# Kernel tuning notes

Measured on AMD Instinct MI355X. Metric: run time of the kernel, lower is better.

## Reference

```python
import jax, jax.numpy as jnp
import numpy as np

N = 20000      # nodes
E = 300000     # edges
HID = 128
HEADS = 4
DH = HID // HEADS
NF = 4         # node_features
EF = 3         # edge_features
NS = 10        # num_servers (Q-head output)
NL = 4         # num_layers


def _ln(h, g, b):
    m = h.mean(-1, keepdims=True)
    v = ((h - m) ** 2).mean(-1, keepdims=True)
    return (h - m) / jnp.sqrt(v + 1e-5) * g + b


def _lrelu(h):
    return jnp.where(h >= 0, h, 0.2 * h)


def setup_inputs() -> dict:
    key = jax.random.key(0)
    ks = jax.random.split(key, 48)
    it = iter(range(48))

    def W(shape, fan_in):
        return jax.random.normal(ks[next(it)], shape, jnp.float32) / np.float32(np.sqrt(fan_in))

    inp = {}
    inp["x"] = jax.random.normal(ks[next(it)], (N, NF), jnp.float32)
    inp["edge_index"] = jax.random.randint(ks[next(it)], (2, E), 0, N)
    inp["edge_attr"] = jax.random.normal(ks[next(it)], (E, EF), jnp.float32)
    # node / edge encoders
    inp["ne_w"] = W((NF, HID), NF); inp["ne_b"] = jnp.zeros((HID,), jnp.float32)
    inp["ne_g"] = jnp.ones((HID,), jnp.float32); inp["ne_beta"] = jnp.zeros((HID,), jnp.float32)
    inp["ee_w"] = W((EF, HID), EF); inp["ee_b"] = jnp.zeros((HID,), jnp.float32)
    inp["ee_g"] = jnp.ones((HID,), jnp.float32); inp["ee_beta"] = jnp.zeros((HID,), jnp.float32)
    # EdgeConv layers (stacked over NL)
    inp["ec_w1"] = W((NL, 2 * HID, HID), 2 * HID); inp["ec_b1"] = jnp.zeros((NL, HID), jnp.float32)
    inp["ec_lng"] = jnp.ones((NL, HID), jnp.float32); inp["ec_lnb"] = jnp.zeros((NL, HID), jnp.float32)
    inp["ec_w2"] = W((NL, HID, HID), HID); inp["ec_b2"] = jnp.zeros((NL, HID), jnp.float32)
    inp["ec_wa"] = W((NL, 2 * HID, 1), 2 * HID); inp["ec_ba"] = jnp.zeros((NL, 1), jnp.float32)
    # GATConv layers
    inp["gat_w"] = W((NL, HID, HID), HID)
    inp["gat_asrc"] = W((NL, HEADS, DH), DH)
    inp["gat_adst"] = W((NL, HEADS, DH), DH)
    inp["gat_bias"] = jnp.zeros((NL, HID), jnp.float32)
    # post-block layer norms
    inp["ln_g"] = jnp.ones((NL, HID), jnp.float32); inp["ln_b"] = jnp.zeros((NL, HID), jnp.float32)
    # dueling heads
    inp["adv_w1"] = W((HID, HID), HID); inp["adv_b1"] = jnp.zeros((HID,), jnp.float32)
    inp["adv_g"] = jnp.ones((HID,), jnp.float32); inp["adv_beta"] = jnp.zeros((HID,), jnp.float32)
    inp["adv_w2"] = W((HID, NS), HID); inp["adv_b2"] = jnp.zeros((NS,), jnp.float32)
    inp["val_w1"] = W((HID, HID), HID); inp["val_b1"] = jnp.zeros((HID,), jnp.float32)
    inp["val_g"] = jnp.ones((HID,), jnp.float32); inp["val_beta"] = jnp.zeros((HID,), jnp.float32)
    inp["val_w2"] = W((HID, 1), HID); inp["val_b2"] = jnp.zeros((1,), jnp.float32)
    return inp


def _forward(x, edge_attr, edge_index,
             ne_w, ne_b, ne_g, ne_beta, ee_w, ee_b, ee_g, ee_beta,
             ec_w1, ec_b1, ec_lng, ec_lnb, ec_w2, ec_b2, ec_wa, ec_ba,
             gat_w, gat_asrc, gat_adst, gat_bias, ln_g, ln_b,
             adv_w1, adv_b1, adv_g, adv_beta, adv_w2, adv_b2,
             val_w1, val_b1, val_g, val_beta, val_w2, val_b2):
    src = edge_index[0]
    dst = edge_index[1]
    h = _ln(_lrelu(x @ ne_w + ne_b), ne_g, ne_beta)                 # node encoder (eval: no dropout)
    _ea = _ln(_lrelu(edge_attr @ ee_w + ee_b), ee_g, ee_beta)        # edge encoder; message() only tests presence
    deg = jax.ops.segment_sum(jnp.ones((E,), h.dtype), dst, num_segments=N)  # in-degree [N]
    sl = jnp.arange(N)
    src_sl = jnp.concatenate([src, sl])                              # GATConv adds self-loops
    dst_sl = jnp.concatenate([dst, sl])

    xc = h
    res = h
    for i in range(NL):
        # ---- EdgeConv: gather-concat, per-edge MLP, sigmoid edge-attention gate, scatter ----
        tmp = jnp.concatenate([xc[dst], xc[src]], axis=1)            # [E, 2H] = x_i || x_j
        m = _lrelu(tmp @ ec_w1[i] + ec_b1[i])
        m = _ln(m, ec_lng[i], ec_lnb[i])
        m = _lrelu(m @ ec_w2[i] + ec_b2[i])
        gate = jax.nn.sigmoid(tmp @ ec_wa[i] + ec_ba[i])             # [E, 1]
        msg = m * gate
        if i % 2 == 0:  # 'max' aggregation (PyG fills isolated nodes with 0)
            agg = jax.ops.segment_max(msg, dst, num_segments=N)
            agg = jnp.where(deg[:, None] > 0, agg, 0.0)
        else:           # 'mean'
            agg = jax.ops.segment_sum(msg, dst, num_segments=N) / jnp.maximum(deg, 1.0)[:, None]
        # ---- GATConv (self-loops, segment softmax over destination) ----
        wx = (xc @ gat_w[i]).reshape(N, HEADS, DH)
        asrc = (wx * gat_asrc[i]).sum(-1)                            # [N, HEADS]
        adst = (wx * gat_adst[i]).sum(-1)
        e = _lrelu(asrc[src_sl] + adst[dst_sl])                      # [E+N, HEADS]
        emax = jax.ops.segment_max(e, dst_sl, num_segments=N)
        p = jnp.exp(e - emax[dst_sl])
        den = jax.ops.segment_sum(p, dst_sl, num_segments=N)
        alpha = p / den[dst_sl]                                      # attention (eval: no dropout)
        gat_out = jax.ops.segment_sum(alpha[:, :, None] * wx[src_sl], dst_sl, num_segments=N)
        gat_out = gat_out.reshape(N, HID) + gat_bias[i]
        # ---- residual + norm + activation ----
        xc = _lrelu(_ln(res + agg + gat_out, ln_g[i], ln_b[i]))
        res = xc

    t = xc[0]                                                        # task node representation
    a = _ln(_lrelu(t @ adv_w1 + adv_b1), adv_g, adv_beta)
    a = a @ adv_w2 + adv_b2                                          # [NS]
    v = _ln(_lrelu(t @ val_w1 + val_b1), val_g, val_beta)
    v = v @ val_w2 + val_b2                                          # [1]
    q = v + (a - a.mean())
    return q, v


def reference(x, edge_index, edge_attr,
              ne_w, ne_b, ne_g, ne_beta, ee_w, ee_b, ee_g, ee_beta,
              ec_w1, ec_b1, ec_lng, ec_lnb, ec_w2, ec_b2, ec_wa, ec_ba,
              gat_w, gat_asrc, gat_adst, gat_bias, ln_g, ln_b,
              adv_w1, adv_b1, adv_g, adv_beta, adv_w2, adv_b2,
              val_w1, val_b1, val_g, val_beta, val_w2, val_b2):
    return _forward(x, edge_attr, edge_index,
                    ne_w, ne_b, ne_g, ne_beta, ee_w, ee_b, ee_g, ee_beta,
                    ec_w1, ec_b1, ec_lng, ec_lnb, ec_w2, ec_b2, ec_wa, ec_ba,
                    gat_w, gat_asrc, gat_adst, gat_bias, ln_g, ln_b,
                    adv_w1, adv_b1, adv_g, adv_beta, adv_w2, adv_b2,
                    val_w1, val_b1, val_g, val_beta, val_w2, val_b2)
```

## Files before the change

kernel.cpp:

```cpp
#include <hip/hip_runtime.h>
#include <hip/hip_bf16.h>

#define NN 20000
#define NE 300000
#define HIDN 128
#define NLAY 4

typedef short short8 __attribute__((ext_vector_type(8)));
typedef float f32x4 __attribute__((ext_vector_type(4)));
typedef unsigned short us16;
typedef unsigned int u32;

__device__ __forceinline__ float lrelu(float x){ return x >= 0.f ? x : 0.2f * x; }
__device__ __forceinline__ float b2f(us16 u){ return __uint_as_float(((u32)u) << 16); }
__device__ __forceinline__ us16 f2b(float f){
    u32 u = __float_as_uint(f);
    u += 0x7FFFu + ((u >> 16) & 1u);
    return (us16)(u >> 16);
}
__device__ __forceinline__ float rawf(const void* p, size_t i, int dt){
    return dt ? b2f(((const us16*)p)[i]) : ((const float*)p)[i];
}
__device__ __forceinline__ int swzi(int i){
    return (i & ~15) | ((i & 15) ^ (((i >> 5) & 3) << 2));
}

__device__ __forceinline__ void ln_stats_128(float v, volatile float* red, float& mean, float& inv){
    float s = v, s2 = v * v;
#pragma unroll
    for (int m = 32; m >= 1; m >>= 1){ s += __shfl_xor(s, m, 64); s2 += __shfl_xor(s2, m, 64); }
    int w = threadIdx.x >> 6;
    if ((threadIdx.x & 63) == 0){ red[w*2] = s; red[w*2+1] = s2; }
    __syncthreads();
    float ts = red[0] + red[2], ts2 = red[1] + red[3];
    mean = ts * (1.f/128.f);
    float var = ts2 * (1.f/128.f) - mean * mean;
    inv = rsqrtf(var + 1e-5f);
    __syncthreads();
}

__global__ void k_detect(const u32* __restrict__ ne_g, int* __restrict__ flag){
    flag[0] = (ne_g[0] == 0x3F803F80u) ? 1 : 0;
}

struct ConvEnt { const void* s; float* d; int n; int pad; };
struct ConvTab { ConvEnt c[28]; int cnt; int pad[3]; };

__global__ void k_convert_all(ConvTab tab, const int* __restrict__ flag){
    int ti = blockIdx.y;
    if (ti >= tab.cnt) return;
    const void* s = tab.c[ti].s;
    float* d = tab.c[ti].d;
    int n = tab.c[ti].n;
    int dt = flag[0];
    for (int i = blockIdx.x*blockDim.x + threadIdx.x; i < n; i += gridDim.x*blockDim.x)
        d[i] = rawf(s, i, dt);
}

#define W1SZ (8*144*32)
#define W2SZ (4*128*32)
#define PER_L (W1SZ + 2*W2SZ)
#define PTOT2 (NLAY*PER_L)
__global__ void k_prepw(const void* __restrict__ ecw1r, const void* __restrict__ ecwar,
                        const void* __restrict__ ecw2r, const void* __restrict__ gatwr,
                        const int* __restrict__ flag,
                        us16* __restrict__ w1s, us16* __restrict__ w2s, us16* __restrict__ gws){
    int id = blockIdx.x*blockDim.x + threadIdx.x;
    if (id >= PTOT2) return;
    int dt = flag[0];
    int L = id / PER_L, r = id % PER_L;
    if (r < W1SZ){
        int kk = r / 4608, rem = r % 4608, n = rem >> 5, ks = rem & 31;
        int k = kk*32 + ks;
        float v;
        if (n < 128)      v = rawf(ecw1r, (size_t)L*32768 + (size_t)k*128 + n, dt);
        else if (n == 128) v = rawf(ecwar, (size_t)L*256 + k, dt);
        else               v = 0.f;
        w1s[(size_t)L*W1SZ + r] = f2b(v);
    } else if (r < W1SZ + W2SZ){
        int rr = r - W1SZ;
        int kk = rr >> 12, rem = rr & 4095, n = rem >> 5, ks = rem & 31;
        int k = kk*32 + ks;
        w2s[(size_t)L*W2SZ + rr] = f2b(rawf(ecw2r, (size_t)L*16384 + (size_t)k*128 + n, dt));
    } else {
        int rr = r - W1SZ - W2SZ;
        int kk = rr >> 12, rem = rr & 4095, n = rem >> 5, ks = rem & 31;
        int k = kk*32 + ks;
        gws[(size_t)L*W2SZ + rr] = f2b(rawf(gatwr, (size_t)L*16384 + (size_t)k*128 + n, dt));
    }
}

__global__ void k_hist(const int* __restrict__ dstI, int* __restrict__ cnt){
    int e = blockIdx.x*blockDim.x + threadIdx.x;
    if (e < NE) atomicAdd(&cnt[dstI[e]], 1);
}
__global__ void k_scan(const int* __restrict__ cnt, int* __restrict__ rowptr){
    __shared__ int ps[256];
    int t = threadIdx.x;
    int chunk = (NN + 255) / 256;
    int beg = t*chunk, end = beg + chunk; if (end > NN) end = NN;
    int s = 0;
    for (int i = beg; i < end; ++i) s += cnt[i];
    ps[t] = s; __syncthreads();
    int off = 0;
    for (int i = 0; i < t; ++i) off += ps[i];
    int run = off;
    for (int i = beg; i < end; ++i){ rowptr[i] = run; run += cnt[i]; }
    if (t == 255) rowptr[NN] = run;
}
__global__ void k_csrfill(const int* __restrict__ srcI, const int* __restrict__ dstI,
                          int* __restrict__ cur, int* __restrict__ perm,
                          int* __restrict__ csr_src){
    int e = blockIdx.x*blockDim.x + threadIdx.x;
    if (e < NE){
        int p = atomicAdd(&cur[dstI[e]], 1);
        perm[e] = p;
        csr_src[p] = srcI[e];
    }
}

__global__ void k_nodeenc(const float* __restrict__ xf, const float* __restrict__ w,
                          const float* __restrict__ b, const float* __restrict__ g,
                          const float* __restrict__ beta, float* __restrict__ h,
                          us16* __restrict__ xb){
    __shared__ float red[4];
    int n = blockIdx.x, t = threadIdx.x;
    float acc = b[t];
#pragma unroll
    for (int k = 0; k < 4; ++k) acc = fmaf(xf[n*4+k], w[k*HIDN+t], acc);
    acc = lrelu(acc);
    float mean, inv; ln_stats_128(acc, red, mean, inv);
    float o = (acc-mean)*inv*g[t] + beta[t];
    h[(size_t)n*HIDN+t] = o;
    xb[(size_t)n*HIDN+t] = f2b(o);
}

__global__ __launch_bounds__(256, 3) void k_edgeconv_mfma(
    const us16* __restrict__ xb, const int* __restrict__ srcI, const int* __restrict__ dstI,
    const us16* __restrict__ w1s, const us16* __restrict__ w2s,
    const float* __restrict__ b1, const float* __restrict__ lng, const float* __restrict__ lnb,
    const float* __restrict__ b2, const float* __restrict__ baP,
    const int* __restrict__ perm, us16* __restrict__ msg)
{
    __shared__ __align__(16) us16 m1s[128*128];
    __shared__ __align__(16) u32 bsl[2][2304];
    int t = threadIdx.x;
    int wv = t >> 6, lane = t & 63, g = lane >> 4, lr = lane & 15;
    int e0 = blockIdx.x * 128;

    u32 offd[2], offs[2];
#pragma unroll
    for (int m = 0; m < 2; ++m){
        int le = e0 + wv*32 + m*16 + lr; if (le >= NE) le = NE - 1;
        offd[m] = (u32)dstI[le] * HIDN;
        offs[m] = (u32)srcI[le] * HIDN;
    }

    const u32* w1u = (const u32*)w1s;
    const u32* w2u = (const u32*)w2s;

    f32x4 acc[2][9];
#pragma unroll
    for (int m = 0; m < 2; ++m)
#pragma unroll
        for (int nt = 0; nt < 9; ++nt) acc[m][nt] = (f32x4)(0.f);

    u32 rS[9];
#pragma unroll
    for (int q = 0; q < 9; ++q) rS[q] = w1u[t + 256*q];
#pragma unroll
    for (int q = 0; q < 9; ++q) bsl[0][swzi(t + 256*q)] = rS[q];
#pragma unroll
    for (int q = 0; q < 9; ++q) rS[q] = w1u[2304 + t + 256*q];
    short8 aCur[2], aNxt[2];
#pragma unroll
    for (int m = 0; m < 2; ++m)
        aCur[m] = *(const short8*)(xb + offd[m] + g*8);
    __syncthreads();

#pragma unroll
    for (int kk = 0; kk < 8; ++kk){
        if (kk < 7){
            int kn = kk + 1;
#pragma unroll
            for (int m = 0; m < 2; ++m)
                aNxt[m] = *(const short8*)(xb + ((kn < 4) ? offd[m] : offs[m]) + (kn&3)*32 + g*8);
        }
        const us16* bp = (const us16*)bsl[kk & 1];
#pragma unroll
        for (int nt = 0; nt < 9; ++nt){
            int row = nt*16 + lr;
            short8 bF = *(const short8*)(bp + row*32 + (g*8 ^ (((row>>1)&3)<<3)));
            acc[0][nt] = __builtin_amdgcn_mfma_f32_16x16x32_bf16(aCur[0], bF, acc[0][nt], 0, 0, 0);
            acc[1][nt] = __builtin_amdgcn_mfma_f32_16x16x32_bf16(aCur[1], bF, acc[1][nt], 0, 0, 0);
        }
        if (kk < 7){
#pragma unroll
            for (int q = 0; q < 9; ++q) bsl[(kk+1)&1][swzi(t + 256*q)] = rS[q];
            if (kk < 6){
#pragma unroll
                for (int q = 0; q < 9; ++q) rS[q] = w1u[(kk+2)*2304 + t + 256*q];
            }
        }
        aCur[0] = aNxt[0]; aCur[1] = aNxt[1];
        __syncthreads();
    }

    float ba = baP[0];
    float ga[2][4];
#pragma unroll
    for (int m = 0; m < 2; ++m)
#pragma unroll
        for (int r = 0; r < 4; ++r){
            float gv = 1.f / (1.f + __expf(-(acc[m][8][r] + ba)));
            ga[m][r] = __shfl(gv, lane & 48, 64);
        }

    float b1v[8], lngv[8], lnbv[8];
#pragma unroll
    for (int nt = 0; nt < 8; ++nt){
        int c = nt*16 + lr;
        b1v[nt] = b1[c]; lngv[nt] = lng[c]; lnbv[nt] = lnb[c];
    }

    u32 rS2[8];
#pragma unroll
    for (int q = 0; q < 8; ++q) rS2[q] = w2u[t + 256*q];

#pragma unroll
    for (int m = 0; m < 2; ++m){
        float m1v[8][4];
        float s1[4] = {0,0,0,0}, s2[4] = {0,0,0,0};
#pragma unroll
        for (int nt = 0; nt < 8; ++nt)
#pragma unroll
            for (int r = 0; r < 4; ++r){
                float v = lrelu(acc[m][nt][r] + b1v[nt]);
                m1v[nt][r] = v; s1[r] += v; s2[r] += v*v;
            }
#pragma unroll
        for (int mk = 8; mk >= 1; mk >>= 1)
#pragma unroll
            for (int r = 0; r < 4; ++r){ s1[r] += __shfl_xor(s1[r], mk, 64); s2[r] += __shfl_xor(s2[r], mk, 64); }
#pragma unroll
        for (int r = 0; r < 4; ++r){
            float mean = s1[r] * (1.f/128.f);
            float var  = s2[r] * (1.f/128.f) - mean*mean;
            float inv  = rsqrtf(var + 1e-5f);
            int row = wv*32 + m*16 + g*4 + r;
            int swz = (row & 7) << 3;
#pragma unroll
            for (int nt = 0; nt < 8; ++nt){
                float v = (m1v[nt][r] - mean)*inv*lngv[nt] + lnbv[nt];
                m1s[row*128 + ((nt*16 + lr) ^ swz)] = f2b(v);
            }
        }
    }
    __syncthreads();
#pragma unroll
    for (int q = 0; q < 8; ++q) bsl[0][swzi(t + 256*q)] = rS2[q];
#pragma unroll
    for (int q = 0; q < 8; ++q) rS2[q] = w2u[2048 + t + 256*q];
    __syncthreads();

    f32x4 acc2[2][8];
#pragma unroll
    for (int m = 0; m < 2; ++m)
#pragma unroll
        for (int nt = 0; nt < 8; ++nt) acc2[m][nt] = (f32x4)(0.f);
#pragma unroll
    for (int kk = 0; kk < 4; ++kk){
        const us16* bp = (const us16*)bsl[kk & 1];
        short8 aF[2];
#pragma unroll
        for (int m = 0; m < 2; ++m){
            int arow = wv*32 + m*16 + lr;
            int aswz = (arow & 7) << 3;
            aF[m] = *(const short8*)(m1s + arow*128 + ((kk*32 + g*8) ^ aswz));
        }
#pragma unroll
        for (int nt = 0; nt < 8; ++nt){
            int row = nt*16 + lr;
            short8 bF = *(const short8*)(bp + row*32 + (g*8 ^ (((row>>1)&3)<<3)));
            acc2[0][nt] = __builtin_amdgcn_mfma_f32_16x16x32_bf16(aF[0], bF, acc2[0][nt], 0, 0, 0);
            acc2[1][nt] = __builtin_amdgcn_mfma_f32_16x16x32_bf16(aF[1], bF, acc2[1][nt], 0, 0, 0);
        }
        if (kk < 3){
#pragma unroll
            for (int q = 0; q < 8; ++q) bsl[(kk+1)&1][swzi(t + 256*q)] = rS2[q];
            if (kk < 2){
#pragma unroll
                for (int q = 0; q < 8; ++q) rS2[q] = w2u[(kk+2)*2048 + t + 256*q];
            }
        }
        __syncthreads();
    }

    float b2v[8];
#pragma unroll
    for (int nt = 0; nt < 8; ++nt) b2v[nt] = b2[nt*16 + lr];
#pragma unroll
    for (int m = 0; m < 2; ++m)
#pragma unroll
        for (int r = 0; r < 4; ++r){
            int row = wv*32 + m*16 + g*4 + r;
            int swz = (row & 7) << 3;
#pragma unroll
            for (int nt = 0; nt < 8; ++nt){
                float v = lrelu(acc2[m][nt][r] + b2v[nt]) * ga[m][r];
                m1s[row*128 + ((nt*16 + lr) ^ swz)] = f2b(v);
            }
        }
    __syncthreads();
    {
        int row = t >> 1, half = t & 1;
        int e = e0 + row;
        if (e < NE){
            size_t ob = (size_t)perm[e] * HIDN;
            int swz = (row & 7) << 3;
#pragma unroll
            for (int q = 0; q < 8; ++q){
                int col = half*64 + q*8;
                *(short8*)(msg + ob + col) = *(const short8*)(m1s + row*128 + (col ^ swz));
            }
        }
    }
}

__global__ __launch_bounds__(256, 4) void k_gatwx(
    const us16* __restrict__ xb, const us16* __restrict__ gws,
    const float* __restrict__ aws, const float* __restrict__ awd,
    us16* __restrict__ wxb, float* __restrict__ asrc, float* __restrict__ adst)
{
    __shared__ __align__(16) us16 sbuf[64*128];
    __shared__ __align__(16) u32 bsl[2][2048];
    int t = threadIdx.x;
    int wv = t >> 6, lane = t & 63, g = lane >> 4, lr = lane & 15;
    int n0 = blockIdx.x * 64;

    int rn = n0 + wv*16 + lr; if (rn >= NN) rn = NN - 1;
    short8 aN[4];
#pragma unroll
    for (int kk = 0; kk < 4; ++kk)
        aN[kk] = *(const short8*)(xb + (size_t)rn*HIDN + kk*32 + g*8);

    const u32* gwu = (const u32*)gws;
    u32 rS[8];
#pragma unroll
    for (int q = 0; q < 8; ++q) rS[q] = gwu[t + 256*q];
#pragma unroll
    for (int q = 0; q < 8; ++q) bsl[0][swzi(t + 256*q)] = rS[q];
#pragma unroll
    for (int q = 0; q < 8; ++q) rS[q] = gwu[2048 + t + 256*q];
    __syncthreads();

    f32x4 acc[8];
#pragma unroll
    for (int i = 0; i < 8; ++i) acc[i] = (f32x4)(0.f);
#pragma unroll
    for (int kk = 0; kk < 4; ++kk){
        const us16* bp = (const us16*)bsl[kk & 1];
#pragma unroll
        for (int nt = 0; nt < 8; ++nt){
            int row = nt*16 + lr;
            short8 bF = *(const short8*)(bp + row*32 + (g*8 ^ (((row>>1)&3)<<3)));
            acc[nt] = __builtin_amdgcn_mfma_f32_16x16x32_bf16(aN[kk], bF, acc[nt], 0, 0, 0);
        }
        if (kk < 3){
#pragma unroll
            for (int q = 0; q < 8; ++q) bsl[(kk+1)&1][swzi(t + 256*q)] = rS[q];
            if (kk < 2){
#pragma unroll
                for (int q = 0; q < 8; ++q) rS[q] = gwu[(kk+2)*2048 + t + 256*q];
            }
        }
        __syncthreads();
    }

    float awsv[8], awdv[8];
#pragma unroll
    for (int nt = 0; nt < 8; ++nt){ awsv[nt] = aws[nt*16 + lr]; awdv[nt] = awd[nt*16 + lr]; }
    float sa[4][4], sd[4][4];
#pragma unroll
    for (int r = 0; r < 4; ++r)
#pragma unroll
        for (int h = 0; h < 4; ++h){
            sa[r][h] = acc[2*h][r]*awsv[2*h] + acc[2*h+1][r]*awsv[2*h+1];
            sd[r][h] = acc[2*h][r]*awdv[2*h] + acc[2*h+1][r]*awdv[2*h+1];
        }
#pragma unroll
    for (int mk = 8; mk >= 1; mk >>= 1)
#pragma unroll
        for (int r = 0; r < 4; ++r)
#pragma unroll
            for (int h = 0; h < 4; ++h){
                sa[r][h] += __shfl_xor(sa[r][h], mk, 64);
                sd[r][h] += __shfl_xor(sd[r][h], mk, 64);
            }
    if (lr == 0){
#pragma unroll
        for (int r = 0; r < 4; ++r){
            int n = n0 + wv*16 + g*4 + r;
            if (n < NN){
                float4 va = make_float4(sa[r][0], sa[r][1], sa[r][2], sa[r][3]);
                float4 vd = make_float4(sd[r][0], sd[r][1], sd[r][2], sd[r][3]);
                *(float4*)(asrc + (size_t)n*4) = va;
                *(float4*)(adst + (size_t)n*4) = vd;
            }
        }
    }

#pragma unroll
    for (int r = 0; r < 4; ++r){
        int row = wv*16 + g*4 + r;
        int swz = (row & 7) << 3;
#pragma unroll
        for (int nt = 0; nt < 8; ++nt)
            sbuf[row*128 + ((nt*16 + lr) ^ swz)] = f2b(acc[nt][r]);
    }
    __syncthreads();
    {
        int row = t >> 2, ch = t & 3;
        int n = n0 + row;
        if (n < NN){
            int swz = (row & 7) << 3;
#pragma unroll
            for (int q = 0; q < 4; ++q){
                int col = ch*32 + q*8;
                *(short8*)(wxb + (size_t)n*HIDN + col) = *(const short8*)(sbuf + row*128 + (col ^ swz));
            }
        }
    }
}

__global__ __launch_bounds__(256, 8) void k_node_update(
    const int* __restrict__ rowptr, const int* __restrict__ csr_src,
    const us16* __restrict__ msg, const us16* __restrict__ wxb,
    const float* __restrict__ asrc, const float* __restrict__ adst,
    const float* __restrict__ xc, const float* __restrict__ gbias,
    const float* __restrict__ lng, const float* __restrict__ lnb,
    float* __restrict__ xout, us16* __restrict__ xbout, int maxmode)
{
    int wv = threadIdx.x >> 6, l = threadIdx.x & 63;
    int n = blockIdx.x*4 + wv;
    if (n >= NN) return;
    int c0 = 2*l, c1 = 2*l + 1;
    int h = l >> 4;

    int b = rowptr[n], en = rowptr[n+1];
    int deg = en - b;

    float adst_h = adst[(size_t)n*4 + h];
    float pself = __expf(fminf(lrelu(asrc[(size_t)n*4 + h] + adst_h), 80.f));
    u32 wq = *(const u32*)(wxb + (size_t)n*HIDN + c0);
    float att0 = pself * b2f((us16)(wq & 0xFFFFu));
    float att1 = pself * b2f((us16)(wq >> 16));
    float den = pself;

    float agg0, agg1;
    if (maxmode){ agg0 = agg1 = -3.0e38f; } else { agg0 = agg1 = 0.f; }

    for (int i = b; i < en; ++i){
        int s = csr_src[i];
        u32 mq = *(const u32*)(msg + (size_t)i*HIDN + c0);
        float m0 = b2f((us16)(mq & 0xFFFFu)), m1 = b2f((us16)(mq >> 16));
        if (maxmode){ agg0 = fmaxf(agg0, m0); agg1 = fmaxf(agg1, m1); }
        else        { agg0 += m0; agg1 += m1; }
        float p = __expf(fminf(lrelu(asrc[(size_t)s*4 + h] + adst_h), 80.f));
        u32 wq2 = *(const u32*)(wxb + (size_t)s*HIDN + c0);
        att0 = fmaf(p, b2f((us16)(wq2 & 0xFFFFu)), att0);
        att1 = fmaf(p, b2f((us16)(wq2 >> 16)), att1);
        den += p;
    }
    float rden = 1.f / den;
    att0 *= rden; att1 *= rden;
    if (maxmode){ if (deg == 0){ agg0 = 0.f; agg1 = 0.f; } }
    else { float rd = 1.f / fmaxf((float)deg, 1.f); agg0 *= rd; agg1 *= rd; }

    float2 xcv = *(const float2*)(xc + (size_t)n*HIDN + c0);
    float s0 = xcv.x + agg0 + att0 + gbias[c0];
    float s1 = xcv.y + agg1 + att1 + gbias[c1];

    float ss = s0 + s1, ss2 = s0*s0 + s1*s1;
#pragma unroll
    for (int mk = 32; mk >= 1; mk >>= 1){ ss += __shfl_xor(ss, mk, 64); ss2 += __shfl_xor(ss2, mk, 64); }
    float mean = ss * (1.f/128.f);
    float var  = ss2 * (1.f/128.f) - mean*mean;
    float inv  = rsqrtf(var + 1e-5f);
    float o0 = lrelu((s0-mean)*inv*lng[c0] + lnb[c0]);
    float o1 = lrelu((s1-mean)*inv*lng[c1] + lnb[c1]);
    *(float2*)(xout + (size_t)n*HIDN + c0) = make_float2(o0, o1);
    u32 pk = (u32)f2b(o0) | ((u32)f2b(o1) << 16);
    *(u32*)(xbout + (size_t)n*HIDN + c0) = pk;
}

__global__ void k_heads(const float* __restrict__ xc,
                        const float* __restrict__ aw1, const float* __restrict__ ab1,
                        const float* __restrict__ ag,  const float* __restrict__ abeta,
                        const float* __restrict__ aw2, const float* __restrict__ ab2,
                        const float* __restrict__ vw1, const float* __restrict__ vb1,
                        const float* __restrict__ vg,  const float* __restrict__ vbeta,
                        const float* __restrict__ vw2, const float* __restrict__ vb2,
                        void* __restrict__ dout, const int* __restrict__ flag){
    __shared__ float red[4];
    __shared__ float ts[128], u1[128], aout[10];
    int t = threadIdx.x;
    ts[t] = xc[t];
    __syncthreads();
    float acc = ab1[t];
    for (int k = 0; k < 128; ++k) acc = fmaf(ts[k], aw1[k*HIDN+t], acc);
    acc = lrelu(acc);
    float mean, inv; ln_stats_128(acc, red, mean, inv);
    u1[t] = (acc-mean)*inv*ag[t] + abeta[t];
    __syncthreads();
    if (t < 10){
        float a = ab2[t];
        for (int k = 0; k < 128; ++k) a = fmaf(u1[k], aw2[k*10+t], a);
        aout[t] = a;
    }
    __syncthreads();
    float accv = vb1[t];
    for (int k = 0; k < 128; ++k) accv = fmaf(ts[k], vw1[k*HIDN+t], accv);
    accv = lrelu(accv);
    float meanv, invv; ln_stats_128(accv, red, meanv, invv);
    float v1 = (accv-meanv)*invv*vg[t] + vbeta[t];
    float pv = v1 * vw2[t];
#pragma unroll
    for (int m = 32; m >= 1; m >>= 1) pv += __shfl_xor(pv, m, 64);
    if ((t & 63) == 0) red[t >> 6] = pv;
    __syncthreads();
    if (t == 0){
        float v = red[0] + red[1] + vb2[0];
        float am = 0.f;
        for (int j = 0; j < 10; ++j) am += aout[j];
        am *= 0.1f;
        int dt = flag[0];
        for (int j = 0; j < 11; ++j){
            float val = (j < 10) ? (v + aout[j] - am) : v;
            if (dt) ((__hip_bfloat16*)dout)[j] = __float2bfloat16(val);
            else    ((float*)dout)[j] = val;
        }
    }
}

extern "C" void kernel_launch(void* const* d_in, const int* in_sizes, int n_in,
                              void* d_out, int out_size, void* d_ws, size_t ws_size,
                              hipStream_t stream)
{
    float* base = (float*)d_ws;
    size_t off = 0;
    auto A = [&](size_t n)->float*{ float* p = base + off; off += (n + 63) & ~(size_t)63; return p; };

    int*   flag   = (int*)A(64);
    float* xf     = A((size_t)NN*4);
    float* new_w  = A(4*HIDN); float* neb = A(HIDN); float* neg_ = A(HIDN); float* nebeta = A(HIDN);
    float* ecb1   = A(NLAY*HIDN);
    float* eclng  = A(NLAY*HIDN); float* eclnb = A(NLAY*HIDN);
    float* ecb2   = A(NLAY*HIDN); float* ecba = A(NLAY);
    float* gasrc  = A(NLAY*HIDN); float* gadst = A(NLAY*HIDN); float* gbias = A(NLAY*HIDN);
    float* lng    = A(NLAY*HIDN); float* lnb = A(NLAY*HIDN);
    float* aw1    = A(HIDN*HIDN); float* ab1 = A(HIDN); float* ag = A(HIDN); float* abeta = A(HIDN);
    float* aw2    = A(HIDN*10);   float* ab2 = A(10);
    float* vw1    = A(HIDN*HIDN); float* vb1 = A(HIDN); float* vg = A(HIDN); float* vbeta = A(HIDN);
    float* vw2    = A(HIDN);      float* vb2 = A(1);
    us16* w1s = (us16*)A((size_t)NLAY*W1SZ/2);
    us16* w2s = (us16*)A((size_t)NLAY*W2SZ/2);
    us16* gws = (us16*)A((size_t)NLAY*W2SZ/2);
    us16* xb   = (us16*)A((size_t)NN*HIDN/2);
    us16* wxb  = (us16*)A((size_t)NN*HIDN/2);
    float* xcA = A((size_t)NN*HIDN);
    float* xcB = A((size_t)NN*HIDN);
    int* cnt     = (int*)A(NN);
    int* rowptr  = (int*)A(NN+1);
    int* cur     = (int*)A(NN);
    int* perm    = (int*)A(NE);
    int* csr_src = (int*)A(NE);
    float* asrc = A(NN*4); float* adst = A(NN*4);
    us16* msg = (us16*)A((size_t)NE*HIDN/2);

    const int* ei   = (const int*)d_in[1];
    const int* srcI = ei;
    const int* dstI = ei + NE;

    k_detect<<<1, 1, 0, stream>>>((const u32*)d_in[5], flag);

    ConvTab tab; int cc = 0;
    auto add = [&](int idx, float* dst, int n){ tab.c[cc].s = d_in[idx]; tab.c[cc].d = dst; tab.c[cc].n = n; tab.c[cc].pad = 0; cc++; };
    add(0,  xf,    NN*4);
    add(3,  new_w, 4*HIDN); add(4, neb, HIDN); add(5, neg_, HIDN); add(6, nebeta, HIDN);
    add(12, ecb1, NLAY*HIDN);
    add(13, eclng, NLAY*HIDN);     add(14, eclnb, NLAY*HIDN);
    add(16, ecb2, NLAY*HIDN);      add(18, ecba, NLAY);
    add(20, gasrc, NLAY*HIDN); add(21, gadst, NLAY*HIDN); add(22, gbias, NLAY*HIDN);
    add(23, lng,   NLAY*HIDN); add(24, lnb, NLAY*HIDN);
    add(25, aw1, HIDN*HIDN); add(26, ab1, HIDN); add(27, ag, HIDN); add(28, abeta, HIDN);
    add(29, aw2, HIDN*10);   add(30, ab2, 10);
    add(31, vw1, HIDN*HIDN); add(32, vb1, HIDN); add(33, vg, HIDN); add(34, vbeta, HIDN);
    add(35, vw2, HIDN);      add(36, vb2, 1);
    tab.cnt = cc;
    dim3 cgrid(64, cc);
    k_convert_all<<<cgrid, 256, 0, stream>>>(tab, flag);

    k_prepw<<<(PTOT2+255)/256, 256, 0, stream>>>(d_in[11], d_in[17], d_in[15], d_in[19],
                                                 flag, w1s, w2s, gws);

    hipMemsetAsync(cnt, 0, NN*sizeof(int), stream);
    k_hist<<<(NE+255)/256, 256, 0, stream>>>(dstI, cnt);
    k_scan<<<1, 256, 0, stream>>>(cnt, rowptr);
    hipMemcpyAsync(cur, rowptr, NN*sizeof(int), hipMemcpyDeviceToDevice, stream);
    k_csrfill<<<(NE+255)/256, 256, 0, stream>>>(srcI, dstI, cur, perm, csr_src);

    k_nodeenc<<<NN, 128, 0, stream>>>(xf, new_w, neb, neg_, nebeta, xcA, xb);

    float* curx = xcA; float* nxt = xcB;
    int eblocks = (NE + 127) / 128;
    int nblocks64 = (NN + 63) / 64;
    int nblocks4  = (NN + 3) / 4;
    for (int i = 0; i < NLAY; ++i){
        int maxmode = (i % 2 == 0);

        k_edgeconv_mfma<<<eblocks, 256, 0, stream>>>(xb, srcI, dstI,
            w1s + (size_t)i*W1SZ, w2s + (size_t)i*W2SZ,
            ecb1 + i*HIDN, eclng + i*HIDN, eclnb + i*HIDN,
            ecb2 + i*HIDN, ecba + i, perm, msg);

        k_gatwx<<<nblocks64, 256, 0, stream>>>(xb, gws + (size_t)i*W2SZ,
            gasrc + i*HIDN, gadst + i*HIDN, wxb, asrc, adst);

        k_node_update<<<nblocks4, 256, 0, stream>>>(rowptr, csr_src, msg, wxb,
            asrc, adst, curx, gbias + i*HIDN, lng + i*HIDN, lnb + i*HIDN,
            nxt, xb, maxmode);

        float* tswap = curx; curx = nxt; nxt = tswap;
    }

    k_heads<<<1, 128, 0, stream>>>(curx, aw1, ab1, ag, abeta, aw2, ab2,
                                   vw1, vb1, vg, vbeta, vw2, vb2, d_out, flag);
}
```

Before: 645.7 us.

## Process edges in CSR order and remap blocks to XCD-contiguous chunks

The edge-conv kernel now walks edges in destination-sorted CSR order, reading precomputed csr_src/csr_dst arrays, and writes messages contiguously instead of scattering them through a perm array. Block IDs are remapped so that each of the 8 XCDs gets a contiguous range of edge blocks, which is meant to improve L2 locality for the gathered destination rows. This removes the scattered msg writes and the perm reads. In exchange, csrfill writes one more array, and the remap hardcodes EBLOCKS=2344 = 8*293.

```diff
diff --git a/kernel.cpp b/kernel.cpp
--- a/kernel.cpp
+++ b/kernel.cpp
@@ -5,6 +5,8 @@
 #define NE 300000
 #define HIDN 128
 #define NLAY 4
+#define EBLOCKS 2344
+#define EB_PER_XCD 293
 
 typedef short short8 __attribute__((ext_vector_type(8)));
 typedef float f32x4 __attribute__((ext_vector_type(4)));
@@ -109,13 +111,14 @@
     if (t == 255) rowptr[NN] = run;
 }
 __global__ void k_csrfill(const int* __restrict__ srcI, const int* __restrict__ dstI,
-                          int* __restrict__ cur, int* __restrict__ perm,
-                          int* __restrict__ csr_src){
+                          int* __restrict__ cur, int* __restrict__ csr_src,
+                          int* __restrict__ csr_dst){
     int e = blockIdx.x*blockDim.x + threadIdx.x;
     if (e < NE){
-        int p = atomicAdd(&cur[dstI[e]], 1);
-        perm[e] = p;
+        int d = dstI[e];
+        int p = atomicAdd(&cur[d], 1);
         csr_src[p] = srcI[e];
+        csr_dst[p] = d;
     }
 }
 
@@ -136,24 +139,26 @@
 }
 
 __global__ __launch_bounds__(256, 3) void k_edgeconv_mfma(
-    const us16* __restrict__ xb, const int* __restrict__ srcI, const int* __restrict__ dstI,
+    const us16* __restrict__ xb, const int* __restrict__ csr_src, const int* __restrict__ csr_dst,
     const us16* __restrict__ w1s, const us16* __restrict__ w2s,
     const float* __restrict__ b1, const float* __restrict__ lng, const float* __restrict__ lnb,
     const float* __restrict__ b2, const float* __restrict__ baP,
-    const int* __restrict__ perm, us16* __restrict__ msg)
+    us16* __restrict__ msg)
 {
     __shared__ __align__(16) us16 m1s[128*128];
     __shared__ __align__(16) u32 bsl[2][2304];
     int t = threadIdx.x;
     int wv = t >> 6, lane = t & 63, g = lane >> 4, lr = lane & 15;
-    int e0 = blockIdx.x * 128;
+    int bid = (int)blockIdx.x;
+    int sb = (bid & 7) * EB_PER_XCD + (bid >> 3);
+    int e0 = sb * 128;
 
     u32 offd[2], offs[2];
 #pragma unroll
     for (int m = 0; m < 2; ++m){
         int le = e0 + wv*32 + m*16 + lr; if (le >= NE) le = NE - 1;
-        offd[m] = (u32)dstI[le] * HIDN;
-        offs[m] = (u32)srcI[le] * HIDN;
+        offd[m] = (u32)csr_dst[le] * HIDN;
+        offs[m] = (u32)csr_src[le] * HIDN;
     }
 
     const u32* w1u = (const u32*)w1s;
@@ -316,7 +321,7 @@
         int row = t >> 1, half = t & 1;
         int e = e0 + row;
         if (e < NE){
-            size_t ob = (size_t)perm[e] * HIDN;
+            size_t ob = (size_t)e * HIDN;
             int swz = (row & 7) << 3;
 #pragma unroll
             for (int q = 0; q < 8; ++q){
@@ -402,10 +407,8 @@
         for (int r = 0; r < 4; ++r){
             int n = n0 + wv*16 + g*4 + r;
             if (n < NN){
-                float4 va = make_float4(sa[r][0], sa[r][1], sa[r][2], sa[r][3]);
-                float4 vd = make_float4(sd[r][0], sd[r][1], sd[r][2], sd[r][3]);
-                *(float4*)(asrc + (size_t)n*4) = va;
-                *(float4*)(adst + (size_t)n*4) = vd;
+                *(float4*)(asrc + (size_t)n*4) = make_float4(sa[r][0], sa[r][1], sa[r][2], sa[r][3]);
+                *(float4*)(adst + (size_t)n*4) = make_float4(sd[r][0], sd[r][1], sd[r][2], sd[r][3]);
             }
         }
     }
@@ -573,8 +576,8 @@
     int* cnt     = (int*)A(NN);
     int* rowptr  = (int*)A(NN+1);
     int* cur     = (int*)A(NN);
-    int* perm    = (int*)A(NE);
     int* csr_src = (int*)A(NE);
+    int* csr_dst = (int*)A(NE);
     float* asrc = A(NN*4); float* adst = A(NN*4);
     us16* msg = (us16*)A((size_t)NE*HIDN/2);
 
@@ -608,21 +611,20 @@
     k_hist<<<(NE+255)/256, 256, 0, stream>>>(dstI, cnt);
     k_scan<<<1, 256, 0, stream>>>(cnt, rowptr);
     hipMemcpyAsync(cur, rowptr, NN*sizeof(int), hipMemcpyDeviceToDevice, stream);
-    k_csrfill<<<(NE+255)/256, 256, 0, stream>>>(srcI, dstI, cur, perm, csr_src);
+    k_csrfill<<<(NE+255)/256, 256, 0, stream>>>(srcI, dstI, cur, csr_src, csr_dst);
 
     k_nodeenc<<<NN, 128, 0, stream>>>(xf, new_w, neb, neg_, nebeta, xcA, xb);
 
     float* curx = xcA; float* nxt = xcB;
-    int eblocks = (NE + 127) / 128;
     int nblocks64 = (NN + 63) / 64;
     int nblocks4  = (NN + 3) / 4;
     for (int i = 0; i < NLAY; ++i){
         int maxmode = (i % 2 == 0);
 
-        k_edgeconv_mfma<<<eblocks, 256, 0, stream>>>(xb, srcI, dstI,
+        k_edgeconv_mfma<<<EBLOCKS, 256, 0, stream>>>(xb, csr_src, csr_dst,
             w1s + (size_t)i*W1SZ, w2s + (size_t)i*W2SZ,
             ecb1 + i*HIDN, eclng + i*HIDN, eclnb + i*HIDN,
-            ecb2 + i*HIDN, ecba + i, perm, msg);
+            ecb2 + i*HIDN, ecba + i, msg);
 
         k_gatwx<<<nblocks64, 256, 0, stream>>>(xb, gws + (size_t)i*W2SZ,
             gasrc + i*HIDN, gadst + i*HIDN, wxb, asrc, adst);
```

New measurement: 637.9 us. No clear change (-1.2%).
